# Kernel optimization log

Hardware: AMD Instinct MI355X
Metric: run time of the kernel (lower is better)

Reference implementation:

```python
import jax, jax.numpy as jnp
import numpy as np

B, N, E, ATT, TT, IT = 32, 5000, 500, 50, 4, 24
TEMP = 0.5

def leaky(x):
    return jnp.where(x > 0, x, 0.1 * x)

def ln(x, g, b, eps=1e-5):
    m = jnp.mean(x, axis=-1, keepdims=True)
    v = jnp.mean((x - m) ** 2, axis=-1, keepdims=True)
    return (x - m) * jax.lax.rsqrt(v + eps) * g + b

def setup_inputs() -> dict:
    key = jax.random.key(0)
    ks = jax.random.split(key, 16)
    s = 0.05
    return {
        'positive_sample': jax.random.randint(ks[0], (B, 3), 0, N),
        'ent_text_emb': jax.random.normal(ks[1], (N, TT, 384), jnp.float32),
        'ent_img_emb': jax.random.normal(ks[2], (N, IT, 383), jnp.float32),
        'entity_embedding': jax.random.normal(ks[3], (N, E), jnp.float32) * s,
        'relation_embedding': jax.random.normal(ks[4], (N, E), jnp.float32) * s,
        'W_text': jax.random.normal(ks[5], (ATT, 384), jnp.float32) * s,
        'b_text': jnp.zeros((ATT,), jnp.float32),
        'W_img': jax.random.normal(ks[6], (ATT, 383), jnp.float32) * s,
        'b_img': jnp.zeros((ATT,), jnp.float32),
        'W_tproj': jax.random.normal(ks[7], (ATT, ATT * IT), jnp.float32) * s,
        'b_tproj': jnp.zeros((ATT,), jnp.float32),
        'W_iproj': jax.random.normal(ks[8], (ATT, ATT * TT), jnp.float32) * s,
        'b_iproj': jnp.zeros((ATT,), jnp.float32),
        'W_rel1': jax.random.normal(ks[9], (IT * TT, E), jnp.float32) * s,
        'b_rel1': jnp.zeros((IT * TT,), jnp.float32),
        'W_rel2': jax.random.normal(ks[10], (IT * TT, E), jnp.float32) * s,
        'b_rel2': jnp.zeros((IT * TT,), jnp.float32),
        'W1': jax.random.normal(ks[11], (100, 2 * E), jnp.float32) * s,
        'b1': jnp.zeros((100,), jnp.float32),
        'W3': jax.random.normal(ks[12], (E, 100), jnp.float32) * s,
        'b3': jnp.zeros((E,), jnp.float32),
        'ln_g': jnp.ones((ATT,), jnp.float32),
        'ln_b': jnp.zeros((ATT,), jnp.float32),
    }

def _cos_sim(X, p):
    # X [B,N,d], p [B,d]; denominators are detached as in the torch code
    num = jnp.einsum('bnd,bd->bn', X, p)
    den = jnp.linalg.norm(X, axis=2) * jnp.linalg.norm(p, axis=1)[:, None]
    return num / (jax.lax.stop_gradient(den) + 1e-10)

def reference(positive_sample, ent_text_emb, ent_img_emb, entity_embedding,
              relation_embedding, W_text, b_text, W_img, b_img, W_tproj, b_tproj,
              W_iproj, b_iproj, W_rel1, b_rel1, W_rel2, b_rel2, W1, b1, W3, b3,
              ln_g, ln_b):
    rel = relation_embedding[positive_sample[:, 1]]              # [B,E]
    text_emb = leaky(jnp.einsum('ntf,df->ntd', ent_text_emb, W_text) + b_text)  # [N,4,50]
    img_emb = leaky(jnp.einsum('nif,df->nid', ent_img_emb, W_img) + b_img)      # [N,24,50]
    cross = jnp.einsum('nid,ntd->nit', img_emb, text_emb)        # [N,24,4]

    # image branch: softmax over img tokens, plus relation-gated path
    img_att = jnp.einsum('nti,nid->ntd', jax.nn.softmax(cross.transpose(0, 2, 1), axis=2), img_emb)  # [N,4,50]
    rg_i = jax.nn.sigmoid(rel @ W_rel1.T + b_rel1).reshape(B, IT, TT)           # [B,24,4]
    gated_i = rg_i[:, None] * cross[None]                                        # [B,N,24,4]
    img_att_rg = jnp.einsum('bnit,nid->bntd', gated_i, img_emb)                  # [B,N,4,50]
    img_att_all = ln(img_att_rg, ln_g, ln_b) + ln(img_att, ln_g, ln_b)[None]
    img_att_all = img_att_all.reshape(B, N, TT * ATT) @ W_iproj.T + b_iproj      # [B,N,50]

    # text branch: softmax over text tokens, plus relation-gated path
    text_att = jnp.einsum('nit,ntd->nid', jax.nn.softmax(cross, axis=2), text_emb)  # [N,24,50]
    rg_t = jax.nn.sigmoid(rel @ W_rel2.T + b_rel2).reshape(B, IT, TT)
    gated_t = rg_t[:, None] * cross[None]                                        # [B,N,24,4]
    text_att_rg = jnp.einsum('bnit,ntd->bnid', gated_t, text_emb)                # [B,N,24,50]
    text_att_all = ln(text_att_rg, ln_g, ln_b) + ln(text_att, ln_g, ln_b)[None]
    text_att_all = text_att_all.reshape(B, N, IT * ATT) @ W_tproj.T + b_tproj    # [B,N,50]

    # structural gate on KGE entity embeddings (split W1 to avoid concat)
    h = leaky(entity_embedding @ W1[:, :E].T[None].squeeze(0).T.T  # placeholder removed below
              ) if False else None
    h = leaky((entity_embedding @ W1[:, :E].T)[None] + (rel @ W1[:, E:].T)[:, None] + b1)  # [B,N,100]
    gate = jax.nn.sigmoid(h @ W3.T + b3)                                         # [B,N,E]
    t_att = entity_embedding[None] * gate                                        # [B,N,E]

    pos_idx = positive_sample[:, 2]  # tail-batch
    bi = jnp.arange(B)
    pos_img = img_att_all[bi, pos_idx]    # [B,50]
    pos_text = text_att_all[bi, pos_idx]  # [B,50]
    pos_t = t_att[bi, pos_idx]            # [B,E]

    simil_img = _cos_sim(img_att_all, pos_img)
    simil_text = _cos_sim(text_att_all, pos_text)
    simil_t = _cos_sim(t_att, pos_t)

    out = (jax.nn.softmax(simil_t / TEMP, axis=1)
           + jax.nn.softmax(simil_img / TEMP, axis=1)
           + jax.nn.softmax(simil_text / TEMP, axis=1))
    return (out, simil_img, simil_text, simil_t)
```

## Files before the change

kernel.cpp:

```cpp
#include <hip/hip_runtime.h>
#include <math.h>

#define BB 32
#define NN 5000
#define EE 500
#define AT 50
#define TTT 4
#define ITT 24
#define FT 384
#define FI 383
#define KH 100
#define BN (BB*NN)

__device__ __forceinline__ float leaky(float x){ return x > 0.f ? x : 0.1f*x; }
__device__ __forceinline__ float sigm(float x){ return 1.f/(1.f+__expf(-x)); }

enum : size_t {
  O_WTT = 0,
  O_WIT = 19968,
  O_WIP = 39936,
  O_WTP = 50336,
  O_W1T = 112736,
  O_W3T = 162736,
  O_SIP = 212736,
  O_STP = 212944,
  O_CBI = 214192,
  O_CBT = 214244,
  O_RGI = 214296,
  O_RGT = 217368,
  O_RB  = 220440,
  O_A   = 223640,
  O_PT  = 723640,
  O_PTN = 739640,
  O_PIM = 739672,
  O_PIMN= 741336,
  O_PTX = 741368,
  O_PTXN= 743032,
  O_MR  = 743064,
  O_SR  = 743160,
  O_EMB = 743256,
};

__global__ void k_prep(const float* Wt, const float* Wi, const float* Wip, const float* Wtp,
                       const float* W1, const float* W3, const float* g, const float* lb,
                       const float* bip, const float* btp, float* ws){
  int id = blockIdx.x*256 + threadIdx.x;
  if (id < 19968){ int f=id/52, d=id%52; ws[O_WTT+id] = (d<50)? Wt[d*FT+f] : 0.f; return; }
  id -= 19968;
  if (id < 19968){ int f=id/52, d=id%52; ws[O_WIT+id] = (f<383 && d<50)? Wi[d*FI+f] : 0.f; return; }
  id -= 19968;
  if (id < 10400){ int m=id/52, o=id%52; int t=m/50, d=m%50;
                   ws[O_WIP+id] = (o<50)? Wip[o*200+t*50+d]*g[d] : 0.f; return; }
  id -= 10400;
  if (id < 62400){ int m=id/52, o=id%52; int i=m/50, d=m%50;
                   ws[O_WTP+id] = (o<50)? Wtp[o*1200+i*50+d]*g[d] : 0.f; return; }
  id -= 62400;
  if (id < 50000){ int e=id/100, k=id%100; ws[O_W1T+id] = W1[k*1000+e]; return; }
  id -= 50000;
  if (id < 50000){ int k=id/500, e=id%500; ws[O_W3T+id] = W3[e*100+k]; return; }
  id -= 50000;
  if (id < 208){ int t=id/52, o=id%52; float s=0;
                 if (o<50) for(int d=0;d<50;d++) s += Wip[o*200+t*50+d]*g[d];
                 ws[O_SIP+id]=s; return; }
  id -= 208;
  if (id < 1248){ int i=id/52, o=id%52; float s=0;
                  if (o<50) for(int d=0;d<50;d++) s += Wtp[o*1200+i*50+d]*g[d];
                  ws[O_STP+id]=s; return; }
  id -= 1248;
  if (id < 52){ int o=id; float s=0;
                if (o<50){ for(int j=0;j<200;j++) s += lb[j%50]*Wip[o*200+j]; s=2.f*s+bip[o]; }
                ws[O_CBI+o]=s; return; }
  id -= 52;
  if (id < 52){ int o=id; float s=0;
                if (o<50){ for(int j=0;j<1200;j++) s += lb[j%50]*Wtp[o*1200+j]; s=2.f*s+btp[o]; }
                ws[O_CBT+o]=s; return; }
}

__global__ void k_rel(const int* ps, const float* rele, const float* Wr1, const float* br1,
                      const float* Wr2, const float* br2, const float* W1, float* ws){
  __shared__ float relL[EE];
  int b = blockIdx.x;
  int r = ps[b*3+1];
  for (int e=threadIdx.x; e<EE; e+=256) relL[e] = rele[(size_t)r*EE+e];
  __syncthreads();
  for (int j=threadIdx.x; j<292; j+=256){
    if (j<96){
      float a=br1[j]; const float* w=&Wr1[j*EE];
      for(int e=0;e<EE;e++) a+=relL[e]*w[e];
      ws[O_RGI+b*96+j]=sigm(a);
    } else if (j<192){
      int jj=j-96; float a=br2[jj]; const float* w=&Wr2[jj*EE];
      for(int e=0;e<EE;e++) a+=relL[e]*w[e];
      ws[O_RGT+b*96+jj]=sigm(a);
    } else {
      int k=j-192; float a=0; const float* w=&W1[k*1000+500];
      for(int e=0;e<EE;e++) a+=relL[e]*w[e];
      ws[O_RB+b*100+k]=a;
    }
  }
}

__global__ void k_A(const float* ent, float* ws){
  __shared__ float entL[8*EE];
  int n0 = blockIdx.x*8;
  for (int idx=threadIdx.x; idx<8*EE; idx+=256) entL[idx] = ent[(size_t)n0*EE + idx];
  __syncthreads();
  const float* W1T = &ws[O_W1T];
  for (int idx=threadIdx.x; idx<800; idx+=256){
    int rr=idx/100, k=idx%100; float a=0;
    const float* el=&entL[rr*EE];
    for (int e=0;e<EE;e++) a += el[e]*W1T[e*100+k];
    ws[O_A + (size_t)k*NN + (n0+rr)] = a;
  }
}

__global__ void k_pos(const int* ps, const float* ent, const float* b1, const float* b3, float* ws){
  __shared__ float hL[KH];
  __shared__ float red[4];
  int b=blockIdx.x; int n=ps[b*3+2]; int tid=threadIdx.x;
  if (tid<KH) hL[tid] = leaky(ws[O_A+(size_t)tid*NN+n] + ws[O_RB+b*100+tid] + b1[tid]);
  __syncthreads();
  const float* w3t=&ws[O_W3T];
  float sq=0;
  for (int e=tid; e<EE; e+=256){
    float a=b3[e];
    for (int k=0;k<KH;k++) a += hL[k]*w3t[k*500+e];
    float gg=sigm(a); float ta=ent[(size_t)n*EE+e]*gg;
    ws[O_PT+b*500+e]=ta; sq+=ta*ta;
  }
  for (int off=1; off<64; off<<=1) sq += __shfl_xor(sq, off);
  if ((tid&63)==0) red[tid>>6]=sq;
  __syncthreads();
  if (tid==0) ws[O_PTN+b] = sqrtf(red[0]+red[1]+red[2]+red[3]);
}

__global__ __launch_bounds__(256) void k_emb(const float* X, const float* Wp, const float* bias,
                                             float* emb, int R, int F, int rowsPerN, int rowOff,
                                             int xstride){
  __shared__ __align__(16) float Wl[128*52];
  int row = blockIdx.x*256 + threadIdx.x;
  bool act = row < R;
  float4 acc[13];
  #pragma unroll
  for (int c=0;c<13;c++) acc[c]=make_float4(0,0,0,0);
  const float* xr = X + (size_t)(act?row:0)*xstride;
  for (int f0=0; f0<F; f0+=128){
    int nf = min(128, F-f0);
    __syncthreads();
    for (int j=threadIdx.x; j<nf*52; j+=256) Wl[j] = Wp[(size_t)f0*52 + j];
    __syncthreads();
    if (act){
      for (int f=0; f<nf; ++f){
        float x = xr[f0+f];
        const float4* wr = (const float4*)&Wl[f*52];
        #pragma unroll
        for (int c=0;c<13;++c){
          float4 w=wr[c];
          acc[c].x+=x*w.x; acc[c].y+=x*w.y; acc[c].z+=x*w.z; acc[c].w+=x*w.w;
        }
      }
    }
  }
  if (act){
    int n = row / rowsPerN, rr = row % rowsPerN;
    float* dst = emb + (size_t)n*1456 + (size_t)(rowOff+rr)*52;
    #pragma unroll
    for (int c=0;c<13;++c){
      float4 v=acc[c]; int o=c*4;
      v.x=leaky(v.x+bias[o]); v.y=leaky(v.y+bias[o+1]);
      if (c<12){ v.z=leaky(v.z+bias[o+2]); v.w=leaky(v.w+bias[o+3]); }
      else { v.z=0.f; v.w=0.f; }
      *(float4*)&dst[o]=v;
    }
  }
}

__global__ __launch_bounds__(256) void k_main(const int* ps, float* ws, float* out, int mode){
  __shared__ __align__(16) float teie[1456];
  __shared__ __align__(16) float Pm[120*52];
  __shared__ __align__(16) float Um[120*32];
  __shared__ __align__(16) float Gi[576];
  __shared__ __align__(16) float crs[96];
  __shared__ __align__(16) float aimg[96], atxt[96];
  __shared__ __align__(16) float part1[96], part2[96];
  __shared__ __align__(16) float aU[120];
  __shared__ __align__(16) float PattC[52], QattC[52];
  __shared__ float Gts[16], mimg[24], mtxt[4];
  __shared__ float muA1[4], muA2[24];
  __shared__ float accD1[32], accN1[32], accD2[32], accN2[32];

  int tid = threadIdx.x;
  int bstar = blockIdx.x;
  int n = mode ? ps[bstar*3+2] : blockIdx.x;

  const float* embn = &ws[O_EMB + (size_t)n*1456];
  for (int j=tid; j<364; j+=256) *(float4*)&teie[j*4] = *(const float4*)&embn[j*4];
  if (tid<32){ accD1[tid]=0.f; accN1[tid]=0.f; accD2[tid]=0.f; accN2[tid]=0.f; }
  __syncthreads();

  for (int it=tid; it<716; it+=256){
    if (it<576){
      int i=it/24, j=it%24; float s=0;
      const float* a=&teie[(4+i)*52]; const float* b=&teie[(4+j)*52];
      for(int d=0;d<50;d++) s+=a[d]*b[d];
      Gi[it]=s;
    } else if (it<672){
      int c=it-576; int i=c>>2, t=c&3; float s=0;
      const float* a=&teie[(4+i)*52]; const float* b=&teie[t*52];
      for(int d=0;d<50;d++) s+=a[d]*b[d];
      crs[c]=s;
    } else if (it<688){
      int c=it-672; int t=c>>2, u=c&3; float s=0;
      const float* a=&teie[t*52]; const float* b=&teie[u*52];
      for(int d=0;d<50;d++) s+=a[d]*b[d];
      Gts[c]=s;
    } else if (it<712){
      int i=it-688; float s=0; const float* a=&teie[(4+i)*52];
      for(int d=0;d<50;d++) s+=a[d];
      mimg[i]=s*0.02f;
    } else {
      int t=it-712; float s=0; const float* a=&teie[t*52];
      for(int d=0;d<50;d++) s+=a[d];
      mtxt[t]=s*0.02f;
    }
  }
  __syncthreads();

  if (tid<4){
    int t=tid;
    float mx=-1e30f; for(int i=0;i<24;i++) mx=fmaxf(mx,crs[i*4+t]);
    float ex[24]; float s=0;
    for(int i=0;i<24;i++){ ex[i]=__expf(crs[i*4+t]-mx); s+=ex[i]; }
    float inv=1.f/s; float mu=0;
    for(int i=0;i<24;i++){ float a=ex[i]*inv; aimg[i*4+t]=a; mu+=a*mimg[i]; }
    muA1[t]=mu;
  } else if (tid>=64 && tid<88){
    int i=tid-64;
    float mx=-1e30f; for(int t=0;t<4;t++) mx=fmaxf(mx,crs[i*4+t]);
    float ex[4]; float s=0;
    for(int t=0;t<4;t++){ ex[t]=__expf(crs[i*4+t]-mx); s+=ex[t]; }
    float inv=1.f/s; float mu=0;
    for(int t=0;t<4;t++){ float a=ex[t]*inv; atxt[i*4+t]=a; mu+=a*mtxt[t]; }
    muA2[i]=mu;
  }
  __syncthreads();

  const float* WIPg=&ws[O_WIP];
  for (int it=tid; it<1248; it+=256){
    int z=it/13, q=it%13; int t=z/24, i=z%24;
    const float* wb=&WIPg[(size_t)(t*50)*52 + q*4];
    const float* ieb=&teie[(4+i)*52];
    float4 a=make_float4(0,0,0,0);
    for (int d=0; d<50; ++d){
      float e=ieb[d];
      float4 w=*(const float4*)&wb[(size_t)d*52];
      a.x+=e*w.x; a.y+=e*w.y; a.z+=e*w.z; a.w+=e*w.w;
    }
    *(float4*)&Pm[z*52+q*4]=a;
  }
  for (int j=tid; j<208; j+=256) Pm[96*52+j]=ws[O_SIP+j];
  if (tid<96){
    int i=tid>>2, t=tid&3;
    float s=0; for(int j=0;j<24;j++) s+=Gi[i*24+j]*aimg[j*4+t];
    part1[tid]=aimg[tid]*s;
  } else if (tid<192){
    int c=tid-96; int t=c&3;
    float s=0; for(int u=0;u<4;u++) s+=Gts[t*4+u]*atxt[(c&~3)+u];
    part2[c]=atxt[c]*s;
  }
  __syncthreads();

  if (tid<128){
    int b=tid&31, t=tid>>5;
    float w1r[24];
    for(int i=0;i<24;i++) w1r[i]=ws[O_RGI+b*96+i*4+t]*crs[i*4+t];
    float mu=0; for(int i=0;i<24;i++) mu+=w1r[i]*mimg[i];
    float q=0;
    for(int i=0;i<24;i++){ float s=0; for(int j=0;j<24;j++) s+=Gi[i*24+j]*w1r[j]; q+=w1r[i]*s; }
    float inv=rsqrtf(q*0.02f-mu*mu+1e-5f);
    for(int i=0;i<24;i++) Um[(t*24+i)*32+b]=inv*w1r[i];
    Um[(96+t)*32+b]=-inv*mu;
  } else if (tid<228){
    int z=tid-128;
    int t=(z<96)? (z/24) : (z-96);
    float q=0; for(int i=0;i<24;i++) q+=part1[i*4+t];
    float inv=rsqrtf(q*0.02f-muA1[t]*muA1[t]+1e-5f);
    aU[z]=(z<96)? inv*aimg[(z%24)*4+t] : -inv*muA1[t];
  }
  __syncthreads();

  if (tid<52){
    float s=ws[O_CBI+tid];
    for(int z=0;z<100;z++) s+=aU[z]*Pm[z*52+tid];
    PattC[tid]=s;
  }
  __syncthreads();

  {
    int b=tid&31, q0=tid>>5;
    bool h2=(q0+8)<13;
    float4 a0=make_float4(0,0,0,0), a1=make_float4(0,0,0,0);
    #pragma unroll 4
    for (int z=0; z<100; ++z){
      float u=Um[z*32+b];
      float4 p0=*(const float4*)&Pm[z*52+q0*4];
      a0.x+=u*p0.x; a0.y+=u*p0.y; a0.z+=u*p0.z; a0.w+=u*p0.w;
      if (h2){
        float4 p1=*(const float4*)&Pm[z*52+(q0+8)*4];
        a1.x+=u*p1.x; a1.y+=u*p1.y; a1.z+=u*p1.z; a1.w+=u*p1.w;
      }
    }
    float4 c0=*(const float4*)&PattC[q0*4];
    a0.x+=c0.x; a0.y+=c0.y; a0.z+=c0.z; a0.w+=c0.w;
    if (h2){ float4 c1=*(const float4*)&PattC[(q0+8)*4]; a1.x+=c1.x; a1.y+=c1.y; a1.z+=c1.z; a1.w+=c1.w; }
    float ni=a0.x*a0.x+a0.y*a0.y+a0.z*a0.z+a0.w*a0.w;
    if (h2) ni+=a1.x*a1.x+a1.y*a1.y+a1.z*a1.z+a1.w*a1.w;
    if (!mode){
      const float* pv=&ws[O_PIM+b*52];
      float4 p0=*(const float4*)&pv[q0*4];
      float di=a0.x*p0.x+a0.y*p0.y+a0.z*p0.z+a0.w*p0.w;
      if (h2){
        float4 p1=*(const float4*)&pv[(q0+8)*4];
        di+=a1.x*p1.x+a1.y*p1.y+a1.z*p1.z+a1.w*p1.w;
      }
      atomicAdd(&accD1[b],di); atomicAdd(&accN1[b],ni);
    } else {
      atomicAdd(&accN1[b],ni);
      if (b==bstar){
        *(float4*)&ws[O_PIM+b*52+q0*4]=a0;
        if (h2) *(float4*)&ws[O_PIM+b*52+(q0+8)*4]=a1;
      }
    }
  }
  __syncthreads();

  if (!mode){
    if (tid<32)
      out[(size_t)BN + (size_t)tid*NN + n] = accD1[tid]/(sqrtf(accN1[tid])*ws[O_PIMN+tid]+1e-10f);
  } else {
    if (tid==0) ws[O_PIMN+bstar]=sqrtf(accN1[bstar]);
  }
  {
    const float* WTPg=&ws[O_WTP];
    for (int it=tid; it<1248; it+=256){
      int z=it/13, q=it%13; int t=z/24, i=z%24;
      const float* wb=&WTPg[(size_t)(i*50)*52 + q*4];
      const float* teb=&teie[t*52];
      float4 a=make_float4(0,0,0,0);
      for (int d=0; d<50; ++d){
        float e=teb[d];
        float4 w=*(const float4*)&wb[(size_t)d*52];
        a.x+=e*w.x; a.y+=e*w.y; a.z+=e*w.z; a.w+=e*w.w;
      }
      *(float4*)&Pm[z*52+q*4]=a;
    }
    for (int j=tid; j<1248; j+=256) Pm[96*52+j]=ws[O_STP+j];
  }
  __syncthreads();

  for (int it=tid; it<888; it+=256){
    if (it<768){
      int b=it&31, i=it>>5;
      float w2r[4];
      for(int t=0;t<4;t++) w2r[t]=ws[O_RGT+b*96+i*4+t]*crs[i*4+t];
      float mu=0; for(int t=0;t<4;t++) mu+=w2r[t]*mtxt[t];
      float q=0;
      for(int t=0;t<4;t++){ float s=0; for(int u=0;u<4;u++) s+=Gts[t*4+u]*w2r[u]; q+=w2r[t]*s; }
      float inv=rsqrtf(q*0.02f-mu*mu+1e-5f);
      for(int t=0;t<4;t++) Um[(t*24+i)*32+b]=inv*w2r[t];
      Um[(96+i)*32+b]=-inv*mu;
    } else {
      int z=it-768;
      int i=(z<96)? (z%24) : (z-96);
      float q=0; for(int t=0;t<4;t++) q+=part2[i*4+t];
      float inv=rsqrtf(q*0.02f-muA2[i]*muA2[i]+1e-5f);
      aU[z]=(z<96)? inv*atxt[(z%24)*4+(z/24)] : -inv*muA2[i];
    }
  }
  __syncthreads();

  if (tid<52){
    float s=ws[O_CBT+tid];
    for(int z=0;z<120;z++) s+=aU[z]*Pm[z*52+tid];
    QattC[tid]=s;
  }
  __syncthreads();

  {
    int b=tid&31, q0=tid>>5;
    bool h2=(q0+8)<13;
    float4 a0=make_float4(0,0,0,0), a1=make_float4(0,0,0,0);
    #pragma unroll 4
    for (int z=0; z<120; ++z){
      float u=Um[z*32+b];
      float4 p0=*(const float4*)&Pm[z*52+q0*4];
      a0.x+=u*p0.x; a0.y+=u*p0.y; a0.z+=u*p0.z; a0.w+=u*p0.w;
      if (h2){
        float4 p1=*(const float4*)&Pm[z*52+(q0+8)*4];
        a1.x+=u*p1.x; a1.y+=u*p1.y; a1.z+=u*p1.z; a1.w+=u*p1.w;
      }
    }
    float4 c0=*(const float4*)&QattC[q0*4];
    a0.x+=c0.x; a0.y+=c0.y; a0.z+=c0.z; a0.w+=c0.w;
    if (h2){ float4 c1=*(const float4*)&QattC[(q0+8)*4]; a1.x+=c1.x; a1.y+=c1.y; a1.z+=c1.z; a1.w+=c1.w; }
    float ni=a0.x*a0.x+a0.y*a0.y+a0.z*a0.z+a0.w*a0.w;
    if (h2) ni+=a1.x*a1.x+a1.y*a1.y+a1.z*a1.z+a1.w*a1.w;
    if (!mode){
      const float* pv=&ws[O_PTX+b*52];
      float4 p0=*(const float4*)&pv[q0*4];
      float di=a0.x*p0.x+a0.y*p0.y+a0.z*p0.z+a0.w*p0.w;
      if (h2){
        float4 p1=*(const float4*)&pv[(q0+8)*4];
        di+=a1.x*p1.x+a1.y*p1.y+a1.z*p1.z+a1.w*p1.w;
      }
      atomicAdd(&accD2[b],di); atomicAdd(&accN2[b],ni);
    } else {
      atomicAdd(&accN2[b],ni);
      if (b==bstar){
        *(float4*)&ws[O_PTX+b*52+q0*4]=a0;
        if (h2) *(float4*)&ws[O_PTX+b*52+(q0+8)*4]=a1;
      }
    }
  }
  __syncthreads();

  if (!mode){
    if (tid<32)
      out[2*(size_t)BN + (size_t)tid*NN + n] = accD2[tid]/(sqrtf(accN2[tid])*ws[O_PTXN+tid]+1e-10f);
  } else {
    if (tid==0) ws[O_PTXN+bstar]=sqrtf(accN2[bstar]);
  }
}

__global__ __launch_bounds__(256) void k_gate(const float* ent, const float* b1, const float* b3,
                                              float* ws, float* out){
  __shared__ __align__(16) float hL[50*68];
  __shared__ __align__(16) float wc[50*128];
  __shared__ __align__(16) float PTb[512];
  __shared__ __align__(16) float b3L[512];
  __shared__ float rbL[KH];

  int tid = threadIdx.x;
  int b   = blockIdx.x & 31;
  int n0  = (blockIdx.x >> 5) * 64;

  for (int j=tid; j<512; j+=256){
    PTb[j] = (j<EE)? ws[O_PT + b*EE + j] : 0.f;
    b3L[j] = (j<EE)? b3[j] : 0.f;
  }
  if (tid < KH) rbL[tid] = ws[O_RB + b*KH + tid] + b1[tid];

  int ej = tid & 31;
  int ni = tid >> 5;

  float pn[8], ps[8];
  #pragma unroll
  for (int r=0;r<8;r++){ pn[r]=0.f; ps[r]=0.f; }

  for (int ec=0; ec<4; ++ec){
    int e0 = ec*128;
    float4 acc[8];
    #pragma unroll
    for (int r=0;r<8;r++) acc[r]=make_float4(0,0,0,0);

    for (int kh=0; kh<2; ++kh){
      __syncthreads();
      for (int idx=tid; idx<1600; idx+=256){
        int k = idx>>5, j4 = idx&31;
        int e = e0 + j4*4;
        float4 v = make_float4(0,0,0,0);
        if (e+3 < EE) v = *(const float4*)&ws[O_W3T + (size_t)(kh*50+k)*EE + e];
        *(float4*)&wc[k*128 + j4*4] = v;
      }
      for (int idx=tid; idx<3200; idx+=256){
        int k = idx>>6, nn = idx&63;
        int n = n0 + nn;
        float v = 0.f;
        if (n < NN) v = leaky(ws[O_A + (size_t)(kh*50+k)*NN + n] + rbL[kh*50+k]);
        hL[k*68 + nn] = v;
      }
      __syncthreads();

      const float4* wp = (const float4*)&wc[ej*4];
      const float4* hp = (const float4*)&hL[ni*8];
      #pragma unroll 2
      for (int k=0;k<50;k++){
        float4 w  = wp[k*32];
        float4 h0 = hp[k*17];
        float4 h1 = hp[k*17 + 1];
        acc[0].x+=h0.x*w.x; acc[0].y+=h0.x*w.y; acc[0].z+=h0.x*w.z; acc[0].w+=h0.x*w.w;
        acc[1].x+=h0.y*w.x; acc[1].y+=h0.y*w.y; acc[1].z+=h0.y*w.z; acc[1].w+=h0.y*w.w;
        acc[2].x+=h0.z*w.x; acc[2].y+=h0.z*w.y; acc[2].z+=h0.z*w.z; acc[2].w+=h0.z*w.w;
        acc[3].x+=h0.w*w.x; acc[3].y+=h0.w*w.y; acc[3].z+=h0.w*w.z; acc[3].w+=h0.w*w.w;
        acc[4].x+=h1.x*w.x; acc[4].y+=h1.x*w.y; acc[4].z+=h1.x*w.z; acc[4].w+=h1.x*w.w;
        acc[5].x+=h1.y*w.x; acc[5].y+=h1.y*w.y; acc[5].z+=h1.y*w.z; acc[5].w+=h1.y*w.w;
        acc[6].x+=h1.z*w.x; acc[6].y+=h1.z*w.y; acc[6].z+=h1.z*w.z; acc[6].w+=h1.z*w.w;
        acc[7].x+=h1.w*w.x; acc[7].y+=h1.w*w.y; acc[7].z+=h1.w*w.z; acc[7].w+=h1.w*w.w;
      }
    }

    {
      int ebase = e0 + ej*4;
      bool ev = (ebase + 3) < EE;
      float4 bb = *(const float4*)&b3L[ebase];
      float4 pt = *(const float4*)&PTb[ebase];
      #pragma unroll
      for (int r=0;r<8;r++){
        int n = n0 + ni*8 + r;
        float4 en = make_float4(0,0,0,0);
        if (ev && n < NN) en = *(const float4*)&ent[(size_t)n*EE + ebase];
        float t0 = en.x * sigm(acc[r].x + bb.x);
        float t1 = en.y * sigm(acc[r].y + bb.y);
        float t2 = en.z * sigm(acc[r].z + bb.z);
        float t3 = en.w * sigm(acc[r].w + bb.w);
        pn[r] += t0*pt.x + t1*pt.y + t2*pt.z + t3*pt.w;
        ps[r] += t0*t0 + t1*t1 + t2*t2 + t3*t3;
      }
    }
  }

  for (int off=1; off<32; off<<=1){
    #pragma unroll
    for (int r=0;r<8;r++){ pn[r]+=__shfl_xor(pn[r],off); ps[r]+=__shfl_xor(ps[r],off); }
  }
  if (ej==0){
    float ptn = ws[O_PTN+b];
    #pragma unroll
    for (int r=0;r<8;r++){
      int n = n0 + ni*8 + r;
      if (n < NN)
        out[3*(size_t)BN + (size_t)b*NN + n] = pn[r]/(sqrtf(ps[r])*ptn + 1e-10f);
    }
  }
}

__global__ void k_smax1(const float* out, float* ws){
  __shared__ float red[4];
  __shared__ float Msh;
  int a=blockIdx.x>>5, b=blockIdx.x&31, tid=threadIdx.x;
  const float* arr=&out[(size_t)(1+a)*BN + (size_t)b*NN];
  float mx=-1e30f;
  for (int i=tid;i<NN;i+=256) mx=fmaxf(mx,arr[i]);
  for (int off=1;off<64;off<<=1) mx=fmaxf(mx,__shfl_xor(mx,off));
  if ((tid&63)==0) red[tid>>6]=mx;
  __syncthreads();
  if (tid==0) Msh=fmaxf(fmaxf(red[0],red[1]),fmaxf(red[2],red[3]));
  __syncthreads();
  float M2=2.f*Msh;
  float s=0;
  for (int i=tid;i<NN;i+=256) s+=__expf(2.f*arr[i]-M2);
  for (int off=1;off<64;off<<=1) s+=__shfl_xor(s,off);
  if ((tid&63)==0) red[tid>>6]=s;
  __syncthreads();
  if (tid==0){ ws[O_MR+a*32+b]=M2; ws[O_SR+a*32+b]=red[0]+red[1]+red[2]+red[3]; }
}

__global__ void k_smax2(float* out, const float* ws){
  int t=blockIdx.x*256+threadIdx.x;
  if (t>=BN) return;
  int b=t/NN;
  float r=0;
  for (int a=0;a<3;a++)
    r += __expf(2.f*out[(size_t)(1+a)*BN+t]-ws[O_MR+a*32+b])/ws[O_SR+a*32+b];
  out[t]=r;
}

extern "C" void kernel_launch(void* const* d_in, const int* in_sizes, int n_in,
                              void* d_out, int out_size, void* d_ws, size_t ws_size,
                              hipStream_t stream){
  (void)in_sizes; (void)n_in; (void)out_size; (void)ws_size;
  const int*   ps  =(const int*)  d_in[0];
  const float* etg =(const float*)d_in[1];
  const float* eig =(const float*)d_in[2];
  const float* ent =(const float*)d_in[3];
  const float* rele=(const float*)d_in[4];
  const float* Wt  =(const float*)d_in[5];
  const float* btx =(const float*)d_in[6];
  const float* Wi  =(const float*)d_in[7];
  const float* bim =(const float*)d_in[8];
  const float* Wtp =(const float*)d_in[9];
  const float* btp =(const float*)d_in[10];
  const float* Wip =(const float*)d_in[11];
  const float* bip =(const float*)d_in[12];
  const float* Wr1 =(const float*)d_in[13];
  const float* br1 =(const float*)d_in[14];
  const float* Wr2 =(const float*)d_in[15];
  const float* br2 =(const float*)d_in[16];
  const float* W1  =(const float*)d_in[17];
  const float* b1  =(const float*)d_in[18];
  const float* W3  =(const float*)d_in[19];
  const float* b3  =(const float*)d_in[20];
  const float* lng =(const float*)d_in[21];
  const float* lnb =(const float*)d_in[22];
  float* ws =(float*)d_ws;
  float* out=(float*)d_out;

  k_prep <<<838,256,0,stream>>>(Wt,Wi,Wip,Wtp,W1,W3,lng,lnb,bip,btp,ws);
  k_rel  <<<32, 256,0,stream>>>(ps,rele,Wr1,br1,Wr2,br2,W1,ws);
  k_A    <<<625,256,0,stream>>>(ent,ws);
  k_pos  <<<32, 256,0,stream>>>(ps,ent,b1,b3,ws);
  k_emb  <<<79, 256,0,stream>>>(etg,&ws[O_WTT],btx,&ws[O_EMB],20000,FT,4,0,FT);
  k_emb  <<<469,256,0,stream>>>(eig,&ws[O_WIT],bim,&ws[O_EMB],120000,FI,24,4,FI);
  k_main <<<32,  256,0,stream>>>(ps,ws,out,1);
  k_main <<<5000,256,0,stream>>>(ps,ws,out,0);
  k_gate <<<32*79,256,0,stream>>>(ent,b1,b3,ws,out);
  k_smax1<<<96, 256,0,stream>>>(out,ws);
  k_smax2<<<625,256,0,stream>>>(out,ws);
}
```

Before: 1.549 ms.

## Register-tile k_main projections, vectorize k_A, double rows per thread in k_emb

Several kernels are reworked together. k_A now reads W1 directly with float4 dot products, so the transposed W1 copy in k_prep goes away. k_emb has each thread accumulate two rows, which halves the grid and shares each shared-memory weight load. In k_main the per-entity projections use a new packed weight layout with register tiles over 6 image tokens or 4 text tokens, and the separate PattC/QattC reduction is folded into the final loop by adding aU to Um. That final loop now handles 4 batches per thread, and the small dot products are vectorized. Register pressure rises, and k_emb occupancy drops because of the larger accumulators and fewer blocks.

```diff
diff --git a/kernel.cpp b/kernel.cpp
--- a/kernel.cpp
+++ b/kernel.cpp
@@ -44,19 +44,20 @@
 __global__ void k_prep(const float* Wt, const float* Wi, const float* Wip, const float* Wtp,
                        const float* W1, const float* W3, const float* g, const float* lb,
                        const float* bip, const float* btp, float* ws){
+  (void)W1;
   int id = blockIdx.x*256 + threadIdx.x;
   if (id < 19968){ int f=id/52, d=id%52; ws[O_WTT+id] = (d<50)? Wt[d*FT+f] : 0.f; return; }
   id -= 19968;
   if (id < 19968){ int f=id/52, d=id%52; ws[O_WIT+id] = (f<383 && d<50)? Wi[d*FI+f] : 0.f; return; }
   id -= 19968;
-  if (id < 10400){ int m=id/52, o=id%52; int t=m/50, d=m%50;
-                   ws[O_WIP+id] = (o<50)? Wip[o*200+t*50+d]*g[d] : 0.f; return; }
+  if (id < 10400){
+    int m=id>>2, c=id&3; int d=m%50, r=m/50; int q=r%13, t=r/13; int o=q*4+c;
+    ws[O_WIP+id] = (o<50)? Wip[o*200+t*50+d]*g[o] : 0.f; return; }
   id -= 10400;
-  if (id < 62400){ int m=id/52, o=id%52; int i=m/50, d=m%50;
-                   ws[O_WTP+id] = (o<50)? Wtp[o*1200+i*50+d]*g[d] : 0.f; return; }
+  if (id < 62400){
+    int m=id>>2, c=id&3; int d=m%50, r=m/50; int q=r%13, i=r/13; int o=q*4+c;
+    ws[O_WTP+id] = (o<50)? Wtp[o*1200+i*50+d]*g[o] : 0.f; return; }
   id -= 62400;
-  if (id < 50000){ int e=id/100, k=id%100; ws[O_W1T+id] = W1[k*1000+e]; return; }
-  id -= 50000;
   if (id < 50000){ int k=id/500, e=id%500; ws[O_W3T+id] = W3[e*100+k]; return; }
   id -= 50000;
   if (id < 208){ int t=id/52, o=id%52; float s=0;
@@ -100,17 +101,22 @@
   }
 }
 
-__global__ void k_A(const float* ent, float* ws){
-  __shared__ float entL[8*EE];
+__global__ void k_A(const float* ent, const float* W1, float* ws){
+  __shared__ __align__(16) float entL[8*EE];
   int n0 = blockIdx.x*8;
-  for (int idx=threadIdx.x; idx<8*EE; idx+=256) entL[idx] = ent[(size_t)n0*EE + idx];
-  __syncthreads();
-  const float* W1T = &ws[O_W1T];
+  for (int idx=threadIdx.x; idx<1000; idx+=256)
+    *(float4*)&entL[idx*4] = *(const float4*)&ent[(size_t)n0*EE + idx*4];
+  __syncthreads();
   for (int idx=threadIdx.x; idx<800; idx+=256){
-    int rr=idx/100, k=idx%100; float a=0;
-    const float* el=&entL[rr*EE];
-    for (int e=0;e<EE;e++) a += el[e]*W1T[e*100+k];
-    ws[O_A + (size_t)k*NN + (n0+rr)] = a;
+    int k=idx>>3, rr=idx&7;
+    const float4* el=(const float4*)&entL[rr*EE];
+    const float4* wr=(const float4*)&W1[(size_t)k*1000];
+    float s=0;
+    for (int e4=0;e4<125;e4++){
+      float4 a=el[e4], w=wr[e4];
+      s += a.x*w.x + a.y*w.y + a.z*w.z + a.w*w.w;
+    }
+    ws[O_A + (size_t)k*NN + (n0+rr)] = s;
   }
 }
 
@@ -138,35 +144,48 @@
                                              float* emb, int R, int F, int rowsPerN, int rowOff,
                                              int xstride){
   __shared__ __align__(16) float Wl[128*52];
-  int row = blockIdx.x*256 + threadIdx.x;
-  bool act = row < R;
-  float4 acc[13];
+  int row0 = blockIdx.x*512 + threadIdx.x;
+  int row1 = row0 + 256;
+  bool act0 = row0 < R, act1 = row1 < R;
+  float4 acc0[13], acc1[13];
   #pragma unroll
-  for (int c=0;c<13;c++) acc[c]=make_float4(0,0,0,0);
-  const float* xr = X + (size_t)(act?row:0)*xstride;
+  for (int c=0;c<13;c++){ acc0[c]=make_float4(0,0,0,0); acc1[c]=make_float4(0,0,0,0); }
+  const float* xr0 = X + (size_t)(act0?row0:0)*xstride;
+  const float* xr1 = X + (size_t)(act1?row1:0)*xstride;
   for (int f0=0; f0<F; f0+=128){
     int nf = min(128, F-f0);
     __syncthreads();
     for (int j=threadIdx.x; j<nf*52; j+=256) Wl[j] = Wp[(size_t)f0*52 + j];
     __syncthreads();
-    if (act){
-      for (int f=0; f<nf; ++f){
-        float x = xr[f0+f];
-        const float4* wr = (const float4*)&Wl[f*52];
-        #pragma unroll
-        for (int c=0;c<13;++c){
-          float4 w=wr[c];
-          acc[c].x+=x*w.x; acc[c].y+=x*w.y; acc[c].z+=x*w.z; acc[c].w+=x*w.w;
-        }
-      }
-    }
-  }
-  if (act){
-    int n = row / rowsPerN, rr = row % rowsPerN;
+    for (int f=0; f<nf; ++f){
+      float x0 = xr0[f0+f], x1 = xr1[f0+f];
+      const float4* wr = (const float4*)&Wl[f*52];
+      #pragma unroll
+      for (int c=0;c<13;++c){
+        float4 w=wr[c];
+        acc0[c].x+=x0*w.x; acc0[c].y+=x0*w.y; acc0[c].z+=x0*w.z; acc0[c].w+=x0*w.w;
+        acc1[c].x+=x1*w.x; acc1[c].y+=x1*w.y; acc1[c].z+=x1*w.z; acc1[c].w+=x1*w.w;
+      }
+    }
+  }
+  if (act0){
+    int n = row0 / rowsPerN, rr = row0 % rowsPerN;
     float* dst = emb + (size_t)n*1456 + (size_t)(rowOff+rr)*52;
     #pragma unroll
     for (int c=0;c<13;++c){
-      float4 v=acc[c]; int o=c*4;
+      float4 v=acc0[c]; int o=c*4;
+      v.x=leaky(v.x+bias[o]); v.y=leaky(v.y+bias[o+1]);
+      if (c<12){ v.z=leaky(v.z+bias[o+2]); v.w=leaky(v.w+bias[o+3]); }
+      else { v.z=0.f; v.w=0.f; }
+      *(float4*)&dst[o]=v;
+    }
+  }
+  if (act1){
+    int n = row1 / rowsPerN, rr = row1 % rowsPerN;
+    float* dst = emb + (size_t)n*1456 + (size_t)(rowOff+rr)*52;
+    #pragma unroll
+    for (int c=0;c<13;++c){
+      float4 v=acc1[c]; int o=c*4;
       v.x=leaky(v.x+bias[o]); v.y=leaky(v.y+bias[o+1]);
       if (c<12){ v.z=leaky(v.z+bias[o+2]); v.w=leaky(v.w+bias[o+3]); }
       else { v.z=0.f; v.w=0.f; }
@@ -184,7 +203,6 @@
   __shared__ __align__(16) float aimg[96], atxt[96];
   __shared__ __align__(16) float part1[96], part2[96];
   __shared__ __align__(16) float aU[120];
-  __shared__ __align__(16) float PattC[52], QattC[52];
   __shared__ float Gts[16], mimg[24], mtxt[4];
   __shared__ float muA1[4], muA2[24];
   __shared__ float accD1[32], accN1[32], accD2[32], accN2[32];
@@ -200,27 +218,42 @@
 
   for (int it=tid; it<716; it+=256){
     if (it<576){
-      int i=it/24, j=it%24; float s=0;
-      const float* a=&teie[(4+i)*52]; const float* b=&teie[(4+j)*52];
-      for(int d=0;d<50;d++) s+=a[d]*b[d];
+      int i=it/24, j=it%24;
+      const float4* a=(const float4*)&teie[(4+i)*52];
+      const float4* b=(const float4*)&teie[(4+j)*52];
+      float s=0;
+      #pragma unroll
+      for(int d=0;d<13;d++){ float4 x=a[d], y=b[d]; s+=x.x*y.x+x.y*y.y+x.z*y.z+x.w*y.w; }
       Gi[it]=s;
     } else if (it<672){
-      int c=it-576; int i=c>>2, t=c&3; float s=0;
-      const float* a=&teie[(4+i)*52]; const float* b=&teie[t*52];
-      for(int d=0;d<50;d++) s+=a[d]*b[d];
+      int c=it-576; int i=c>>2, t=c&3;
+      const float4* a=(const float4*)&teie[(4+i)*52];
+      const float4* b=(const float4*)&teie[t*52];
+      float s=0;
+      #pragma unroll
+      for(int d=0;d<13;d++){ float4 x=a[d], y=b[d]; s+=x.x*y.x+x.y*y.y+x.z*y.z+x.w*y.w; }
       crs[c]=s;
     } else if (it<688){
-      int c=it-672; int t=c>>2, u=c&3; float s=0;
-      const float* a=&teie[t*52]; const float* b=&teie[u*52];
-      for(int d=0;d<50;d++) s+=a[d]*b[d];
+      int c=it-672; int t=c>>2, u=c&3;
+      const float4* a=(const float4*)&teie[t*52];
+      const float4* b=(const float4*)&teie[u*52];
+      float s=0;
+      #pragma unroll
+      for(int d=0;d<13;d++){ float4 x=a[d], y=b[d]; s+=x.x*y.x+x.y*y.y+x.z*y.z+x.w*y.w; }
       Gts[c]=s;
     } else if (it<712){
-      int i=it-688; float s=0; const float* a=&teie[(4+i)*52];
-      for(int d=0;d<50;d++) s+=a[d];
+      int i=it-688;
+      const float4* a=(const float4*)&teie[(4+i)*52];
+      float s=0;
+      #pragma unroll
+      for(int d=0;d<13;d++){ float4 x=a[d]; s+=x.x+x.y+x.z+x.w; }
       mimg[i]=s*0.02f;
     } else {
-      int t=it-712; float s=0; const float* a=&teie[t*52];
-      for(int d=0;d<50;d++) s+=a[d];
+      int t=it-712;
+      const float4* a=(const float4*)&teie[t*52];
+      float s=0;
+      #pragma unroll
+      for(int d=0;d<13;d++){ float4 x=a[d]; s+=x.x+x.y+x.z+x.w; }
       mtxt[t]=s*0.02f;
     }
   }
@@ -245,39 +278,81 @@
   }
   __syncthreads();
 
-  const float* WIPg=&ws[O_WIP];
-  for (int it=tid; it<1248; it+=256){
-    int z=it/13, q=it%13; int t=z/24, i=z%24;
-    const float* wb=&WIPg[(size_t)(t*50)*52 + q*4];
-    const float* ieb=&teie[(4+i)*52];
-    float4 a=make_float4(0,0,0,0);
-    for (int d=0; d<50; ++d){
-      float e=ieb[d];
-      float4 w=*(const float4*)&wb[(size_t)d*52];
-      a.x+=e*w.x; a.y+=e*w.y; a.z+=e*w.z; a.w+=e*w.w;
-    }
-    *(float4*)&Pm[z*52+q*4]=a;
-  }
-  for (int j=tid; j<208; j+=256) Pm[96*52+j]=ws[O_SIP+j];
-  if (tid<96){
-    int i=tid>>2, t=tid&3;
-    float s=0; for(int j=0;j<24;j++) s+=Gi[i*24+j]*aimg[j*4+t];
-    part1[tid]=aimg[tid]*s;
-  } else if (tid<192){
-    int c=tid-96; int t=c&3;
-    float s=0; for(int u=0;u<4;u++) s+=Gts[t*4+u]*atxt[(c&~3)+u];
-    part2[c]=atxt[c]*s;
+  if (tid<208){
+    int ig=tid&3, r=tid>>2, q=r%13, t=r/13;
+    const float* wb = &ws[O_WIP + (size_t)(t*13+q)*200];
+    const float* eb = &teie[(4+ig*6)*52];
+    float4 acc[6];
+    #pragma unroll
+    for (int l=0;l<6;l++) acc[l]=make_float4(0,0,0,0);
+    for (int dc=0; dc<12; ++dc){
+      float e[6][4];
+      #pragma unroll
+      for (int l=0;l<6;l++){
+        float4 v=*(const float4*)&eb[l*52+dc*4];
+        e[l][0]=v.x; e[l][1]=v.y; e[l][2]=v.z; e[l][3]=v.w;
+      }
+      #pragma unroll
+      for (int dd=0; dd<4; ++dd){
+        float4 w=*(const float4*)&wb[(dc*4+dd)*4];
+        #pragma unroll
+        for (int l=0;l<6;l++){
+          acc[l].x+=e[l][dd]*w.x; acc[l].y+=e[l][dd]*w.y;
+          acc[l].z+=e[l][dd]*w.z; acc[l].w+=e[l][dd]*w.w;
+        }
+      }
+    }
+    #pragma unroll
+    for (int d=48; d<50; ++d){
+      float4 w=*(const float4*)&wb[d*4];
+      #pragma unroll
+      for (int l=0;l<6;l++){
+        float ee=eb[l*52+d];
+        acc[l].x+=ee*w.x; acc[l].y+=ee*w.y; acc[l].z+=ee*w.z; acc[l].w+=ee*w.w;
+      }
+    }
+    #pragma unroll
+    for (int l=0;l<6;l++) *(float4*)&Pm[(t*24+ig*6+l)*52 + q*4]=acc[l];
+  } else {
+    for (int c=tid-208; c<244; c+=48){
+      if (c<96){
+        int i=c>>2, t=c&3;
+        float s=0; for(int j=0;j<24;j++) s+=Gi[i*24+j]*aimg[j*4+t];
+        part1[c]=aimg[c]*s;
+      } else if (c<192){
+        int cc=c-96; int t=cc&3;
+        float s=0; for(int u=0;u<4;u++) s+=Gts[t*4+u]*atxt[(cc&~3)+u];
+        part2[cc]=atxt[cc]*s;
+      } else {
+        int j=c-192;
+        *(float4*)&Pm[96*52+j*4] = *(const float4*)&ws[O_SIP+j*4];
+      }
+    }
   }
   __syncthreads();
 
   if (tid<128){
     int b=tid&31, t=tid>>5;
     float w1r[24];
+    #pragma unroll
     for(int i=0;i<24;i++) w1r[i]=ws[O_RGI+b*96+i*4+t]*crs[i*4+t];
-    float mu=0; for(int i=0;i<24;i++) mu+=w1r[i]*mimg[i];
+    float mu=0;
+    #pragma unroll
+    for(int i=0;i<24;i++) mu+=w1r[i]*mimg[i];
     float q=0;
-    for(int i=0;i<24;i++){ float s=0; for(int j=0;j<24;j++) s+=Gi[i*24+j]*w1r[j]; q+=w1r[i]*s; }
+    #pragma unroll
+    for(int i=0;i<24;i++){
+      const float4* gr=(const float4*)&Gi[i*24];
+      float s=0;
+      #pragma unroll
+      for(int j4=0;j4<6;j4++){
+        float4 g=gr[j4];
+        s+=g.x*w1r[j4*4]+g.y*w1r[j4*4+1]+g.z*w1r[j4*4+2]+g.w*w1r[j4*4+3];
+      }
+      q+=w1r[i]*s;
+    }
     float inv=rsqrtf(q*0.02f-mu*mu+1e-5f);
+    #pragma unroll
     for(int i=0;i<24;i++) Um[(t*24+i)*32+b]=inv*w1r[i];
     Um[(96+t)*32+b]=-inv*mu;
   } else if (tid<228){
@@ -289,46 +364,49 @@
   }
   __syncthreads();
 
-  if (tid<52){
-    float s=ws[O_CBI+tid];
-    for(int z=0;z<100;z++) s+=aU[z]*Pm[z*52+tid];
-    PattC[tid]=s;
-  }
-  __syncthreads();
-
-  {
-    int b=tid&31, q0=tid>>5;
-    bool h2=(q0+8)<13;
+  if (tid<104){
+    int bg=tid/13, q=tid-bg*13;
     float4 a0=make_float4(0,0,0,0), a1=make_float4(0,0,0,0);
-    #pragma unroll 4
+    float4 a2=make_float4(0,0,0,0), a3=make_float4(0,0,0,0);
     for (int z=0; z<100; ++z){
-      float u=Um[z*32+b];
-      float4 p0=*(const float4*)&Pm[z*52+q0*4];
-      a0.x+=u*p0.x; a0.y+=u*p0.y; a0.z+=u*p0.z; a0.w+=u*p0.w;
-      if (h2){
-        float4 p1=*(const float4*)&Pm[z*52+(q0+8)*4];
-        a1.x+=u*p1.x; a1.y+=u*p1.y; a1.z+=u*p1.z; a1.w+=u*p1.w;
-      }
-    }
-    float4 c0=*(const float4*)&PattC[q0*4];
-    a0.x+=c0.x; a0.y+=c0.y; a0.z+=c0.z; a0.w+=c0.w;
-    if (h2){ float4 c1=*(const float4*)&PattC[(q0+8)*4]; a1.x+=c1.x; a1.y+=c1.y; a1.z+=c1.z; a1.w+=c1.w; }
-    float ni=a0.x*a0.x+a0.y*a0.y+a0.z*a0.z+a0.w*a0.w;
-    if (h2) ni+=a1.x*a1.x+a1.y*a1.y+a1.z*a1.z+a1.w*a1.w;
+      float az=aU[z];
+      float4 u=*(const float4*)&Um[z*32+bg*4];
+      float4 p=*(const float4*)&Pm[z*52+q*4];
+      float u0=u.x+az, u1=u.y+az, u2=u.z+az, u3=u.w+az;
+      a0.x+=u0*p.x; a0.y+=u0*p.y; a0.z+=u0*p.z; a0.w+=u0*p.w;
+      a1.x+=u1*p.x; a1.y+=u1*p.y; a1.z+=u1*p.z; a1.w+=u1*p.w;
+      a2.x+=u2*p.x; a2.y+=u2*p.y; a2.z+=u2*p.z; a2.w+=u2*p.w;
+      a3.x+=u3*p.x; a3.y+=u3*p.y; a3.z+=u3*p.z; a3.w+=u3*p.w;
+    }
+    float4 cb=*(const float4*)&ws[O_CBI+q*4];
+    a0.x+=cb.x; a0.y+=cb.y; a0.z+=cb.z; a0.w+=cb.w;
+    a1.x+=cb.x; a1.y+=cb.y; a1.z+=cb.z; a1.w+=cb.w;
+    a2.x+=cb.x; a2.y+=cb.y; a2.z+=cb.z; a2.w+=cb.w;
+    a3.x+=cb.x; a3.y+=cb.y; a3.z+=cb.z; a3.w+=cb.w;
+    float n0=a0.x*a0.x+a0.y*a0.y+a0.z*a0.z+a0.w*a0.w;
+    float n1=a1.x*a1.x+a1.y*a1.y+a1.z*a1.z+a1.w*a1.w;
+    float n2=a2.x*a2.x+a2.y*a2.y+a2.z*a2.z+a2.w*a2.w;
+    float n3=a3.x*a3.x+a3.y*a3.y+a3.z*a3.z+a3.w*a3.w;
+    int b0=bg*4;
     if (!mode){
-      const float* pv=&ws[O_PIM+b*52];
-      float4 p0=*(const float4*)&pv[q0*4];
-      float di=a0.x*p0.x+a0.y*p0.y+a0.z*p0.z+a0.w*p0.w;
-      if (h2){
-        float4 p1=*(const float4*)&pv[(q0+8)*4];
-        di+=a1.x*p1.x+a1.y*p1.y+a1.z*p1.z+a1.w*p1.w;
-      }
-      atomicAdd(&accD1[b],di); atomicAdd(&accN1[b],ni);
+      const float* PV=&ws[O_PIM];
+      float4 p0=*(const float4*)&PV[(b0+0)*52+q*4];
+      float4 p1=*(const float4*)&PV[(b0+1)*52+q*4];
+      float4 p2=*(const float4*)&PV[(b0+2)*52+q*4];
+      float4 p3=*(const float4*)&PV[(b0+3)*52+q*4];
+      atomicAdd(&accD1[b0+0], a0.x*p0.x+a0.y*p0.y+a0.z*p0.z+a0.w*p0.w);
+      atomicAdd(&accD1[b0+1], a1.x*p1.x+a1.y*p1.y+a1.z*p1.z+a1.w*p1.w);
+      atomicAdd(&accD1[b0+2], a2.x*p2.x+a2.y*p2.y+a2.z*p2.z+a2.w*p2.w);
+      atomicAdd(&accD1[b0+3], a3.x*p3.x+a3.y*p3.y+a3.z*p3.z+a3.w*p3.w);
+      atomicAdd(&accN1[b0+0],n0); atomicAdd(&accN1[b0+1],n1);
+      atomicAdd(&accN1[b0+2],n2); atomicAdd(&accN1[b0+3],n3);
     } else {
-      atomicAdd(&accN1[b],ni);
-      if (b==bstar){
-        *(float4*)&ws[O_PIM+b*52+q0*4]=a0;
-        if (h2) *(float4*)&ws[O_PIM+b*52+(q0+8)*4]=a1;
+      atomicAdd(&accN1[b0+0],n0); atomicAdd(&accN1[b0+1],n1);
+      atomicAdd(&accN1[b0+2],n2); atomicAdd(&accN1[b0+3],n3);
+      if ((bstar>>2)==bg){
+        int bl=bstar&3;
+        float4 sel = (bl==0)? a0 : (bl==1)? a1 : (bl==2)? a2 : a3;
+        *(float4*)&ws[O_PIM+(size_t)bstar*52+q*4]=sel;
       }
     }
   }
@@ -340,21 +418,52 @@
   } else {
     if (tid==0) ws[O_PIMN+bstar]=sqrtf(accN1[bstar]);
   }
-  {
-    const float* WTPg=&ws[O_WTP];
-    for (int it=tid; it<1248; it+=256){
-      int z=it/13, q=it%13; int t=z/24, i=z%24;
-      const float* wb=&WTPg[(size_t)(i*50)*52 + q*4];
-      const float* teb=&teie[t*52];
-      float4 a=make_float4(0,0,0,0);
-      for (int d=0; d<50; ++d){
-        float e=teb[d];
-        float4 w=*(const float4*)&wb[(size_t)d*52];
-        a.x+=e*w.x; a.y+=e*w.y; a.z+=e*w.z; a.w+=e*w.w;
-      }
-      *(float4*)&Pm[z*52+q*4]=a;
-    }
-    for (int j=tid; j<1248; j+=256) Pm[96*52+j]=ws[O_STP+j];
+  if (tid<156){
+    int q=tid%13, i2=tid/13;
+    const float* wbA = &ws[O_WTP + (size_t)((i2*2+0)*13+q)*200];
+    const float* wbB = &ws[O_WTP + (size_t)((i2*2+1)*13+q)*200];
+    float4 accA[4], accB[4];
+    #pragma unroll
+    for (int t=0;t<4;t++){ accA[t]=make_float4(0,0,0,0); accB[t]=make_float4(0,0,0,0); }
+    for (int dc=0; dc<12; ++dc){
+      float e[4][4];
+      #pragma unroll
+      for (int t=0;t<4;t++){
+        float4 v=*(const float4*)&teie[t*52+dc*4];
+        e[t][0]=v.x; e[t][1]=v.y; e[t][2]=v.z; e[t][3]=v.w;
+      }
+      #pragma unroll
+      for (int dd=0; dd<4; ++dd){
+        float4 wA=*(const float4*)&wbA[(dc*4+dd)*4];
+        float4 wB=*(const float4*)&wbB[(dc*4+dd)*4];
+        #pragma unroll
+        for (int t=0;t<4;t++){
+          accA[t].x+=e[t][dd]*wA.x; accA[t].y+=e[t][dd]*wA.y;
+          accA[t].z+=e[t][dd]*wA.z; accA[t].w+=e[t][dd]*wA.w;
+          accB[t].x+=e[t][dd]*wB.x; accB[t].y+=e[t][dd]*wB.y;
+          accB[t].z+=e[t][dd]*wB.z; accB[t].w+=e[t][dd]*wB.w;
+        }
+      }
+    }
+    #pragma unroll
+    for (int d=48; d<50; ++d){
+      float4 wA=*(const float4*)&wbA[d*4];
+      float4 wB=*(const float4*)&wbB[d*4];
+      #pragma unroll
+      for (int t=0;t<4;t++){
+        float ee=teie[t*52+d];
+        accA[t].x+=ee*wA.x; accA[t].y+=ee*wA.y; accA[t].z+=ee*wA.z; accA[t].w+=ee*wA.w;
+        accB[t].x+=ee*wB.x; accB[t].y+=ee*wB.y; accB[t].z+=ee*wB.z; accB[t].w+=ee*wB.w;
+      }
+    }
+    #pragma unroll
+    for (int t=0;t<4;t++){
+      *(float4*)&Pm[(t*24+i2*2+0)*52 + q*4]=accA[t];
+      *(float4*)&Pm[(t*24+i2*2+1)*52 + q*4]=accB[t];
+    }
+  } else {
+    for (int j=tid-156; j<312; j+=100)
+      *(float4*)&Pm[96*52+j*4] = *(const float4*)&ws[O_STP+j*4];
   }
   __syncthreads();
 
@@ -362,11 +471,21 @@
     if (it<768){
       int b=it&31, i=it>>5;
       float w2r[4];
+      #pragma unroll
       for(int t=0;t<4;t++) w2r[t]=ws[O_RGT+b*96+i*4+t]*crs[i*4+t];
-      float mu=0; for(int t=0;t<4;t++) mu+=w2r[t]*mtxt[t];
+      float mu=0;
+      #pragma unroll
+      for(int t=0;t<4;t++) mu+=w2r[t]*mtxt[t];
       float q=0;
-      for(int t=0;t<4;t++){ float s=0; for(int u=0;u<4;u++) s+=Gts[t*4+u]*w2r[u]; q+=w2r[t]*s; }
+      #pragma unroll
+      for(int t=0;t<4;t++){
+        float s=0;
+        #pragma unroll
+        for(int u=0;u<4;u++) s+=Gts[t*4+u]*w2r[u];
+        q+=w2r[t]*s;
+      }
       float inv=rsqrtf(q*0.02f-mu*mu+1e-5f);
+      #pragma unroll
       for(int t=0;t<4;t++) Um[(t*24+i)*32+b]=inv*w2r[t];
       Um[(96+i)*32+b]=-inv*mu;
     } else {
@@ -379,46 +498,49 @@
   }
   __syncthreads();
 
-  if (tid<52){
-    float s=ws[O_CBT+tid];
-    for(int z=0;z<120;z++) s+=aU[z]*Pm[z*52+tid];
-    QattC[tid]=s;
-  }
-  __syncthreads();
-
-  {
-    int b=tid&31, q0=tid>>5;
-    bool h2=(q0+8)<13;
+  if (tid<104){
+    int bg=tid/13, q=tid-bg*13;
     float4 a0=make_float4(0,0,0,0), a1=make_float4(0,0,0,0);
-    #pragma unroll 4
+    float4 a2=make_float4(0,0,0,0), a3=make_float4(0,0,0,0);
     for (int z=0; z<120; ++z){
-      float u=Um[z*32+b];
-      float4 p0=*(const float4*)&Pm[z*52+q0*4];
-      a0.x+=u*p0.x; a0.y+=u*p0.y; a0.z+=u*p0.z; a0.w+=u*p0.w;
-      if (h2){
-        float4 p1=*(const float4*)&Pm[z*52+(q0+8)*4];
-        a1.x+=u*p1.x; a1.y+=u*p1.y; a1.z+=u*p1.z; a1.w+=u*p1.w;
-      }
-    }
-    float4 c0=*(const float4*)&QattC[q0*4];
-    a0.x+=c0.x; a0.y+=c0.y; a0.z+=c0.z; a0.w+=c0.w;
-    if (h2){ float4 c1=*(const float4*)&QattC[(q0+8)*4]; a1.x+=c1.x; a1.y+=c1.y; a1.z+=c1.z; a1.w+=c1.w; }
-    float ni=a0.x*a0.x+a0.y*a0.y+a0.z*a0.z+a0.w*a0.w;
-    if (h2) ni+=a1.x*a1.x+a1.y*a1.y+a1.z*a1.z+a1.w*a1.w;
+      float az=aU[z];
+      float4 u=*(const float4*)&Um[z*32+bg*4];
+      float4 p=*(const float4*)&Pm[z*52+q*4];
+      float u0=u.x+az, u1=u.y+az, u2=u.z+az, u3=u.w+az;
+      a0.x+=u0*p.x; a0.y+=u0*p.y; a0.z+=u0*p.z; a0.w+=u0*p.w;
+      a1.x+=u1*p.x; a1.y+=u1*p.y; a1.z+=u1*p.z; a1.w+=u1*p.w;
+      a2.x+=u2*p.x; a2.y+=u2*p.y; a2.z+=u2*p.z; a2.w+=u2*p.w;
+      a3.x+=u3*p.x; a3.y+=u3*p.y; a3.z+=u3*p.z; a3.w+=u3*p.w;
+    }
+    float4 cb=*(const float4*)&ws[O_CBT+q*4];
+    a0.x+=cb.x; a0.y+=cb.y; a0.z+=cb.z; a0.w+=cb.w;
+    a1.x+=cb.x; a1.y+=cb.y; a1.z+=cb.z; a1.w+=cb.w;
+    a2.x+=cb.x; a2.y+=cb.y; a2.z+=cb.z; a2.w+=cb.w;
+    a3.x+=cb.x; a3.y+=cb.y; a3.z+=cb.z; a3.w+=cb.w;
+    float n0=a0.x*a0.x+a0.y*a0.y+a0.z*a0.z+a0.w*a0.w;
+    float n1=a1.x*a1.x+a1.y*a1.y+a1.z*a1.z+a1.w*a1.w;
+    float n2=a2.x*a2.x+a2.y*a2.y+a2.z*a2.z+a2.w*a2.w;
+    float n3=a3.x*a3.x+a3.y*a3.y+a3.z*a3.z+a3.w*a3.w;
+    int b0=bg*4;
     if (!mode){
-      const float* pv=&ws[O_PTX+b*52];
-      float4 p0=*(const float4*)&pv[q0*4];
-      float di=a0.x*p0.x+a0.y*p0.y+a0.z*p0.z+a0.w*p0.w;
-      if (h2){
-        float4 p1=*(const float4*)&pv[(q0+8)*4];
-        di+=a1.x*p1.x+a1.y*p1.y+a1.z*p1.z+a1.w*p1.w;
-      }
-      atomicAdd(&accD2[b],di); atomicAdd(&accN2[b],ni);
+      const float* PV=&ws[O_PTX];
+      float4 p0=*(const float4*)&PV[(b0+0)*52+q*4];
+      float4 p1=*(const float4*)&PV[(b0+1)*52+q*4];
+      float4 p2=*(const float4*)&PV[(b0+2)*52+q*4];
+      float4 p3=*(const float4*)&PV[(b0+3)*52+q*4];
+      atomicAdd(&accD2[b0+0], a0.x*p0.x+a0.y*p0.y+a0.z*p0.z+a0.w*p0.w);
+      atomicAdd(&accD2[b0+1], a1.x*p1.x+a1.y*p1.y+a1.z*p1.z+a1.w*p1.w);
+      atomicAdd(&accD2[b0+2], a2.x*p2.x+a2.y*p2.y+a2.z*p2.z+a2.w*p2.w);
+      atomicAdd(&accD2[b0+3], a3.x*p3.x+a3.y*p3.y+a3.z*p3.z+a3.w*p3.w);
+      atomicAdd(&accN2[b0+0],n0); atomicAdd(&accN2[b0+1],n1);
+      atomicAdd(&accN2[b0+2],n2); atomicAdd(&accN2[b0+3],n3);
     } else {
-      atomicAdd(&accN2[b],ni);
-      if (b==bstar){
-        *(float4*)&ws[O_PTX+b*52+q0*4]=a0;
-        if (h2) *(float4*)&ws[O_PTX+b*52+(q0+8)*4]=a1;
+      atomicAdd(&accN2[b0+0],n0); atomicAdd(&accN2[b0+1],n1);
+      atomicAdd(&accN2[b0+2],n2); atomicAdd(&accN2[b0+3],n3);
+      if ((bstar>>2)==bg){
+        int bl=bstar&3;
+        float4 sel = (bl==0)? a0 : (bl==1)? a1 : (bl==2)? a2 : a3;
+        *(float4*)&ws[O_PTX+(size_t)bstar*52+q*4]=sel;
       }
     }
   }
@@ -595,12 +717,12 @@
   float* ws =(float*)d_ws;
   float* out=(float*)d_out;
 
-  k_prep <<<838,256,0,stream>>>(Wt,Wi,Wip,Wtp,W1,W3,lng,lnb,bip,btp,ws);
+  k_prep <<<642,256,0,stream>>>(Wt,Wi,Wip,Wtp,W1,W3,lng,lnb,bip,btp,ws);
   k_rel  <<<32, 256,0,stream>>>(ps,rele,Wr1,br1,Wr2,br2,W1,ws);
-  k_A    <<<625,256,0,stream>>>(ent,ws);
+  k_A    <<<625,256,0,stream>>>(ent,W1,ws);
   k_pos  <<<32, 256,0,stream>>>(ps,ent,b1,b3,ws);
-  k_emb  <<<79, 256,0,stream>>>(etg,&ws[O_WTT],btx,&ws[O_EMB],20000,FT,4,0,FT);
-  k_emb  <<<469,256,0,stream>>>(eig,&ws[O_WIT],bim,&ws[O_EMB],120000,FI,24,4,FI);
+  k_emb  <<<40, 256,0,stream>>>(etg,&ws[O_WTT],btx,&ws[O_EMB],20000,FT,4,0,FT);
+  k_emb  <<<235,256,0,stream>>>(eig,&ws[O_WIT],bim,&ws[O_EMB],120000,FI,24,4,FI);
   k_main <<<32,  256,0,stream>>>(ps,ws,out,1);
   k_main <<<5000,256,0,stream>>>(ps,ws,out,0);
   k_gate <<<32*79,256,0,stream>>>(ent,b1,b3,ws,out);
```

Result: slower. 1.666 ms (+7.5%).
